# Kernel tuning notes

Measured on AMD Instinct MI355X. Metric: run time of the kernel, lower is better.

Reference implementation:

```python
import jax, jax.numpy as jnp
import numpy as np
from jax import lax

B, Z, X, Y = 8, 4, 32, 32
N = Z * X * Y
REAL_SIZE = jnp.array([25.0, 25.0, 4.0], dtype=jnp.float32)
THRESHOLD = 0.5
CUTOFF = 2.0


def setup_inputs() -> dict:
    key = jax.random.key(0)
    k1, k2 = jax.random.split(key)
    pred = jax.random.normal(k1, (B, Z, X, Y, 10), dtype=jnp.float32)
    targ = jax.random.uniform(k2, (B, Z, X, Y, 10), dtype=jnp.float32)
    return {"pred": pred, "targ": targ}


def _grid():
    z, x, y = jnp.meshgrid(jnp.arange(Z), jnp.arange(X), jnp.arange(Y), indexing="ij")
    return jnp.stack([z, x, y], -1).reshape(N, 3).astype(jnp.float32)


def _nms_mask(adj0, a0):
    # Fixed-size masked version of the original iterative suppression:
    # adj0: [N,N] bool, strictly-upper-triangular 'closer than cutoff' graph
    # a0:   [N] bool, currently active (above-threshold) points in conf-desc order
    def step(state):
        a, _ = state
        m = adj0 & a[:, None] & a[None, :]
        mf = m.astype(jnp.float32)
        r = mf.sum(0)                              # restrain_tensor = DIS.sum(0)
        r = r - (r != 0).astype(jnp.float32) @ mf  # subtract suppressed suppressors
        return ((r == 0.0) & a, a.sum())
    def cond(state):
        a, prev = state
        return a.sum() != prev
    a, _ = lax.while_loop(cond, step, (a0, jnp.int32(-1)))
    return a


def _per_batch(pd_conf, pd_pos, pd_R, tg_conf, tg_pos, tg_R):
    # pd_conf/tg_conf: [N]; pd_pos/tg_pos: [N,3] normalized; pd_R/tg_R: [N,3,3]
    pd_active = pd_conf > THRESHOLD
    tg_active = tg_conf > THRESHOLD
    # sort predictions by confidence descending, inactive pushed to the end
    skey = jnp.where(pd_active, pd_conf, -jnp.inf)
    order = jnp.argsort(-skey)
    pd_pos = pd_pos[order]
    pd_R = pd_R[order]
    a0 = pd_active[order]
    # NMS in NORMALIZED coordinates (as in the original module: real_size scaling
    # is applied only AFTER argnms)
    d = jnp.sqrt(jnp.sum((pd_pos[:, None, :] - pd_pos[None, :, :]) ** 2, -1))  # [N,N]
    iu = jnp.arange(N)
    adj0 = (d < CUTOFF) & (iu[:, None] < iu[None, :])
    keep = lax.stop_gradient(_nms_mask(adj0, a0))
    # greedy matching in real coordinates
    pd_r = pd_pos * REAL_SIZE
    tg_r = tg_pos * REAL_SIZE
    dist = jnp.sqrt(jnp.sum((tg_r[:, None, :] - pd_r[None, :, :]) ** 2, -1))  # [N_tg, N_pd]
    within = (dist < CUTOFF) & tg_active[:, None] & keep[None, :]
    has = within.any(0)                 # pred j has at least one target within cutoff
    first_tg = jnp.argmax(within, 0)    # first (lowest-index) matching target per pred
    tp = has.sum().astype(jnp.int32)
    n_pd = keep.sum().astype(jnp.int32)
    n_tg = tg_active.sum().astype(jnp.int32)
    cm = jnp.stack([tp, n_pd - tp, n_tg - tp])  # [matched, unmatched_pred, unmatched_targ]
    # mean rotation-angle error over matched pairs (3 rotation rows each)
    tgRm = tg_R[first_tg]  # [N,3,3]
    cos = jnp.sum(pd_R * tgRm, -1) / (
        jnp.linalg.norm(pd_R, axis=-1) * jnp.linalg.norm(tgRm, axis=-1))
    ang = jnp.arccos(jnp.clip(cos, -1.0, 1.0)) / jnp.pi * 180.0  # [N,3]
    w = has.astype(jnp.float32)[:, None]
    ms = jnp.where(tp > 0,
                   jnp.sum(ang * w) / (3.0 * jnp.maximum(tp, 1).astype(jnp.float32)),
                   0.0)
    return cm, ms


def _forward(pred, targ):
    grid = _grid()
    zxy = jnp.array([Z, X, Y], dtype=jnp.float32)
    def fields(t, is_pred):
        conf = jax.nn.sigmoid(t[..., 0]) if is_pred else t[..., 0]
        conf = conf.reshape(B, N)
        pos = (t[..., 1:4].reshape(B, N, 3) + grid) / zxy  # (off + cell_idx)/ZXY
        rx = t[..., 4:7].reshape(B, N, 3)
        ry = t[..., 7:10].reshape(B, N, 3)
        R = jnp.stack([rx, ry, jnp.cross(rx, ry)], axis=-2)  # [B,N,3,3]
        return conf, pos, R
    pc, pp, pR = fields(pred, True)
    tc, tpos, tR = fields(targ, False)
    cm, ms = jax.vmap(_per_batch)(pc, pp, pR, tc, tpos, tR)
    return cm.reshape(B, 1, 1, 3), ms.reshape(B, 1, 1, 1).astype(jnp.float32)


def reference(pred, targ):
    return _forward(pred, targ)
```

## Files before the change

### kernel.cpp

```cpp
#include <hip/hip_runtime.h>
#include <math.h>

#define NB    8
#define NPTS  4096
#define NTH   1024
#define SPT   4
#define NFILT 16
#define MAXQ  64
#define MAXU  256
#define MAXK  256

#define WS_PCNT 0
#define WS_TCNT 32
#define WS_PKEY 4096
#define WS_PPOS 266240
#define WS_TPOS 790528

__device__ __forceinline__ int blockReduceSumI(int v, int* scr, int tid) {
    #pragma unroll
    for (int o = 32; o > 0; o >>= 1) v += __shfl_down(v, o, 64);
    if ((tid & 63) == 0) scr[tid >> 6] = v;
    __syncthreads();
    if (tid == 0) {
        int s = 0;
        #pragma unroll
        for (int w = 0; w < NTH / 64; ++w) s += scr[w];
        scr[16] = s;
    }
    __syncthreads();
    return scr[16];
}

__device__ __forceinline__ float blockReduceSumF(float v, float* scr, int tid) {
    #pragma unroll
    for (int o = 32; o > 0; o >>= 1) v += __shfl_down(v, o, 64);
    if ((tid & 63) == 0) scr[tid >> 6] = v;
    __syncthreads();
    if (tid == 0) {
        float s = 0.0f;
        #pragma unroll
        for (int w = 0; w < NTH / 64; ++w) s += scr[w];
        scr[16] = s;
    }
    __syncthreads();
    return scr[16];
}

__device__ __forceinline__ float rowAngleDeg(float a0, float a1, float a2,
                                             float b0, float b1, float b2) {
    float dot = a0 * b0 + a1 * b1 + a2 * b2;
    float na = sqrtf(a0 * a0 + a1 * a1 + a2 * a2);
    float nb = sqrtf(b0 * b0 + b1 * b1 + b2 * b2);
    float c = dot / (na * nb);
    c = fminf(1.0f, fmaxf(-1.0f, c));
    return acosf(c) * 57.29577951308232f;
}

__global__ __launch_bounds__(256) void prep_kernel(const float* __restrict__ pred,
                                                   const float* __restrict__ targ,
                                                   unsigned char* __restrict__ ws) {
    __shared__ int lcnt;
    __shared__ int gbase;
    __shared__ int wbase[4];
    unsigned int* pcnt = (unsigned int*)(ws + WS_PCNT);
    unsigned int* tcnt = (unsigned int*)(ws + WS_TCNT);
    unsigned long long* pkey = (unsigned long long*)(ws + WS_PKEY);
    float4* ppos = (float4*)(ws + WS_PPOS);
    float4* tpos = (float4*)(ws + WS_TPOS);

    const int tid = threadIdx.x;
    const int g = blockIdx.x * 256 + tid;
    const int tensor = g >> 15;
    const int batch = (g >> 12) & 7;
    const int n = g & 4095;
    const float* base = (tensor ? targ : pred)
                        + (size_t)batch * NPTS * 10 + (size_t)n * 10;
    float2 f0 = *(const float2*)base;
    float2 f1 = *(const float2*)(base + 2);
    float gz = (float)(n >> 10);
    float gx = (float)((n >> 5) & 31);
    float gy = (float)(n & 31);

    bool active;
    unsigned long long key = 0;
    float4 rec;
    if (tensor == 0) {
        float conf = 1.0f / (1.0f + expf(-f0.x));
        active = conf > 0.5f;
        unsigned int u = ~(__float_as_uint(conf) | 0x80000000u);
        key = ((unsigned long long)u << 32) | (unsigned int)n;
        rec = make_float4((f0.y + gz) * 0.25f,
                          (f1.x + gx) * 0.03125f,
                          (f1.y + gy) * 0.03125f,
                          (float)n);
    } else {
        active = f0.x > 0.5f;
        rec = make_float4((f0.y + gz) * 0.25f * 25.0f,
                          (f1.x + gx) * 0.03125f * 25.0f,
                          (f1.y + gy) * 0.03125f * 4.0f,
                          (float)n);
    }

    if (tid == 0) lcnt = 0;
    __syncthreads();
    const int lane = tid & 63, wid = tid >> 6;
    unsigned long long ball = __ballot(active);
    int lofs = __popcll(ball & ((1ull << lane) - 1ull));
    if (lane == 0) wbase[wid] = atomicAdd(&lcnt, __popcll(ball));
    __syncthreads();
    if (tid == 0) {
        unsigned int* cp = tensor ? &tcnt[batch] : &pcnt[batch];
        gbase = (int)atomicAdd(cp, (unsigned int)lcnt);
    }
    __syncthreads();
    if (active) {
        int e = batch * NPTS + gbase + wbase[wid] + lofs;
        if (tensor == 0) { pkey[e] = key; ppos[e] = rec; }
        else tpos[e] = rec;
    }
}

__global__ __launch_bounds__(NTH) void molan_kernel(const float* __restrict__ pred,
                                                    const float* __restrict__ targ,
                                                    const unsigned char* __restrict__ ws,
                                                    float* __restrict__ out) {
    __shared__ int   scr_i[32];
    __shared__ float scr_f[32];
    __shared__ unsigned long long scr_m[16];
    __shared__ int   cnt[8];
    __shared__ unsigned long long f_key[NFILT];
    __shared__ float f_x[NFILT], f_y[NFILT], f_z[NFILT];
    __shared__ unsigned long long q_key[MAXQ];
    __shared__ float q_x[MAXQ], q_y[MAXQ], q_z[MAXQ];
    __shared__ unsigned long long u_key[MAXU];
    __shared__ float u_x[MAXU], u_y[MAXU], u_z[MAXU];
    __shared__ float k_x[MAXK], k_y[MAXK], k_z[MAXK];
    __shared__ int   k_idx[MAXK];
    __shared__ unsigned int k_match[MAXK];

    const int b = blockIdx.x;
    const int tid = threadIdx.x;
    const float* pb = pred + (size_t)b * NPTS * 10;
    const float* tb = targ + (size_t)b * NPTS * 10;
    const unsigned int* pcnt = (const unsigned int*)(ws + WS_PCNT);
    const unsigned int* tcnt = (const unsigned int*)(ws + WS_TCNT);
    const unsigned long long* pkey = (const unsigned long long*)(ws + WS_PKEY) + b * NPTS;
    const float4* ppos = (const float4*)(ws + WS_PPOS) + b * NPTS;
    const float4* tpos = (const float4*)(ws + WS_TPOS) + b * NPTS;
    const int np = (int)pcnt[b];
    const int nt = (int)tcnt[b];

    unsigned long long key[SPT];
    bool  act[SPT];
    int   pidx[SPT];
    float cx[SPT], cy[SPT], cz[SPT];
    #pragma unroll
    for (int s = 0; s < SPT; ++s) {
        int slot = tid + NTH * s;
        bool a = slot < np;
        act[s] = a;
        key[s] = a ? pkey[slot] : ~0ull;
        float4 p = a ? ppos[slot] : make_float4(0.f, 0.f, 0.f, 0.f);
        cx[s] = p.x; cy[s] = p.y; cz[s] = p.z; pidx[s] = (int)p.w;
    }
    bool  t_act[SPT];
    int   t_n[SPT];
    float t_x[SPT], t_y[SPT], t_z[SPT];
    #pragma unroll
    for (int s = 0; s < SPT; ++s) {
        int slot = tid + NTH * s;
        bool a = slot < nt;
        t_act[s] = a;
        float4 p = a ? tpos[slot] : make_float4(0.f, 0.f, 0.f, 0.f);
        t_x[s] = p.x; t_y[s] = p.y; t_z[s] = p.z; t_n[s] = (int)p.w;
    }

    int cur = np;
    int prev = -1;
    while (cur != prev) {
        {
            unsigned long long bk = ~0ull;
            float bx = 0.f, by = 0.f, bz = 0.f;
            #pragma unroll
            for (int s = 0; s < SPT; ++s)
                if (act[s] && key[s] < bk) { bk = key[s]; bx = cx[s]; by = cy[s]; bz = cz[s]; }
            #pragma unroll
            for (int o = 32; o > 0; o >>= 1) {
                unsigned long long ok = __shfl_xor(bk, o, 64);
                float ox = __shfl_xor(bx, o, 64);
                float oy = __shfl_xor(by, o, 64);
                float oz = __shfl_xor(bz, o, 64);
                if (ok < bk) { bk = ok; bx = ox; by = oy; bz = oz; }
            }
            if ((tid & 63) == 0) {
                int w = tid >> 6;
                f_key[w] = bk; f_x[w] = bx; f_y[w] = by; f_z[w] = bz;
            }
        }
        __syncthreads();

        bool sflag[SPT], pend[SPT];
        #pragma unroll
        for (int s = 0; s < SPT; ++s) {
            sflag[s] = false; pend[s] = false;
            if (!act[s]) continue;
            bool found = false;
            for (int f = 0; f < NFILT; ++f) {
                if (f_key[f] < key[s]) {
                    float dx = f_x[f] - cx[s], dy = f_y[f] - cy[s], dz = f_z[f] - cz[s];
                    if (dx * dx + dy * dy + dz * dz < 4.0f) { found = true; break; }
                }
            }
            if (found) sflag[s] = true;
            else pend[s] = true;
        }
        while (true) {
            if (tid == 0) cnt[1] = 0;
            __syncthreads();
            int qe[SPT];
            #pragma unroll
            for (int s = 0; s < SPT; ++s) {
                qe[s] = -1;
                if (pend[s]) {
                    int e = atomicAdd(&cnt[1], 1);
                    if (e < MAXQ) {
                        q_key[e] = key[s]; q_x[e] = cx[s]; q_y[e] = cy[s]; q_z[e] = cz[s];
                        qe[s] = e; pend[s] = false;
                    }
                }
            }
            __syncthreads();
            if (cnt[1] == 0) break;
            const int Q = min(cnt[1], MAXQ);
            unsigned long long mask = 0;
            for (int e = 0; e < Q; ++e) {
                unsigned long long qk = q_key[e];
                float qx = q_x[e], qy = q_y[e], qz = q_z[e];
                bool hit = false;
                #pragma unroll
                for (int s = 0; s < SPT; ++s) {
                    if (act[s] && key[s] < qk) {
                        float dx = cx[s] - qx, dy = cy[s] - qy, dz = cz[s] - qz;
                        if (dx * dx + dy * dy + dz * dz < 4.0f) hit = true;
                    }
                }
                if (hit) mask |= (1ull << e);
            }
            #pragma unroll
            for (int o = 32; o > 0; o >>= 1) mask |= __shfl_xor(mask, o, 64);
            if ((tid & 63) == 0) scr_m[tid >> 6] = mask;
            __syncthreads();
            unsigned long long full = 0;
            #pragma unroll
            for (int w = 0; w < NTH / 64; ++w) full |= scr_m[w];
            #pragma unroll
            for (int s = 0; s < SPT; ++s)
                if (qe[s] >= 0) sflag[s] = (full >> qe[s]) & 1ull;
        }

        bool upend[SPT], supp[SPT];
        #pragma unroll
        for (int s = 0; s < SPT; ++s) {
            upend[s] = act[s] && !sflag[s];
            supp[s] = false;
        }
        while (true) {
            if (tid == 0) cnt[2] = 0;
            __syncthreads();
            #pragma unroll
            for (int s = 0; s < SPT; ++s) {
                if (upend[s]) {
                    int e = atomicAdd(&cnt[2], 1);
                    if (e < MAXU) {
                        u_key[e] = key[s]; u_x[e] = cx[s]; u_y[e] = cy[s]; u_z[e] = cz[s];
                        upend[s] = false;
                    }
                }
            }
            __syncthreads();
            if (cnt[2] == 0) break;
            const int Ku = min(cnt[2], MAXU);
            #pragma unroll
            for (int s = 0; s < SPT; ++s) {
                if (!act[s] || supp[s]) continue;
                for (int e = 0; e < Ku; ++e) {
                    if (u_key[e] < key[s]) {
                        float dx = u_x[e] - cx[s], dy = u_y[e] - cy[s], dz = u_z[e] - cz[s];
                        if (dx * dx + dy * dy + dz * dz < 4.0f) { supp[s] = true; break; }
                    }
                }
            }
        }
        int loc = 0;
        #pragma unroll
        for (int s = 0; s < SPT; ++s) {
            if (act[s] && supp[s]) act[s] = false;
            loc += act[s] ? 1 : 0;
        }
        prev = cur;
        cur = blockReduceSumI(loc, scr_i, tid);
    }
    const int n_pd = cur;

    bool kpend[SPT];
    #pragma unroll
    for (int s = 0; s < SPT; ++s) kpend[s] = act[s];
    int loc_tp = 0;
    float loc_ang = 0.0f;
    while (true) {
        if (tid == 0) cnt[3] = 0;
        __syncthreads();
        #pragma unroll
        for (int s = 0; s < SPT; ++s) {
            if (kpend[s]) {
                int e = atomicAdd(&cnt[3], 1);
                if (e < MAXK) {
                    k_x[e] = cx[s] * 25.0f; k_y[e] = cy[s] * 25.0f; k_z[e] = cz[s] * 4.0f;
                    k_idx[e] = pidx[s];
                    k_match[e] = 0xFFFFFFFFu;
                    kpend[s] = false;
                }
            }
        }
        __syncthreads();
        if (cnt[3] == 0) break;
        const int K = min(cnt[3], MAXK);
        #pragma unroll
        for (int s = 0; s < SPT; ++s) {
            if (!t_act[s]) continue;
            float tx = t_x[s], ty = t_y[s], tz = t_z[s];
            for (int e = 0; e < K; ++e) {
                float dx = tx - k_x[e], dy = ty - k_y[e], dz = tz - k_z[e];
                if (dx * dx + dy * dy + dz * dz < 4.0f)
                    atomicMin(&k_match[e], (unsigned int)t_n[s]);
            }
        }
        __syncthreads();
        if (tid < K) {
            unsigned int m = k_match[tid];
            if (m != 0xFFFFFFFFu) {
                ++loc_tp;
                const float2* pr = (const float2*)(pb + (size_t)k_idx[tid] * 10 + 4);
                float2 p0 = pr[0], p1 = pr[1], p2v = pr[2];
                float ax0 = p0.x, ax1 = p0.y, ax2 = p1.x;
                float ay0 = p1.y, ay1 = p2v.x, ay2 = p2v.y;
                float az0 = ax1 * ay2 - ax2 * ay1;
                float az1 = ax2 * ay0 - ax0 * ay2;
                float az2 = ax0 * ay1 - ax1 * ay0;
                const float2* tr = (const float2*)(tb + (size_t)m * 10 + 4);
                float2 t0 = tr[0], t1 = tr[1], t2v = tr[2];
                float bx0 = t0.x, bx1 = t0.y, bx2 = t1.x;
                float by0 = t1.y, by1 = t2v.x, by2 = t2v.y;
                float bz0 = bx1 * by2 - bx2 * by1;
                float bz1 = bx2 * by0 - bx0 * by2;
                float bz2 = bx0 * by1 - bx1 * by0;
                loc_ang += rowAngleDeg(ax0, ax1, ax2, bx0, bx1, bx2);
                loc_ang += rowAngleDeg(ay0, ay1, ay2, by0, by1, by2);
                loc_ang += rowAngleDeg(az0, az1, az2, bz0, bz1, bz2);
            }
        }
    }

    int tp = blockReduceSumI(loc_tp, scr_i, tid);
    float angsum = blockReduceSumF(loc_ang, scr_f, tid);

    if (tid == 0) {
        out[b * 3 + 0] = (float)tp;
        out[b * 3 + 1] = (float)(n_pd - tp);
        out[b * 3 + 2] = (float)(nt - tp);
        out[NB * 3 + b] = (tp > 0) ? (angsum / (3.0f * (float)tp)) : 0.0f;
    }
}

extern "C" void kernel_launch(void* const* d_in, const int* in_sizes, int n_in,
                              void* d_out, int out_size, void* d_ws, size_t ws_size,
                              hipStream_t stream) {
    const float* pred = (const float*)d_in[0];
    const float* targ = (const float*)d_in[1];
    float* out = (float*)d_out;
    unsigned char* ws = (unsigned char*)d_ws;
    hipMemsetAsync(ws, 0, 64, stream);
    prep_kernel<<<dim3(256), dim3(256), 0, stream>>>(pred, targ, ws);
    molan_kernel<<<dim3(NB), dim3(NTH), 0, stream>>>(pred, targ, ws, out);
}
```

Measured before the change: 79.34 us.

## Replace global atomic compaction with per-chunk counts and drop the memset

The prep kernel now writes per-256-point chunk counts instead of atomically appending to global per-batch counters, so the separate memset launch and the atomics go away. The main kernel reads the 16 chunk counts per batch and treats slots as a sparse chunked layout rather than a dense prefix. It also raises the query buffer size, replaces the ballot mask reduction with a shared result array, and turns the batch loops into do-while loops that exit after a single pass when counts fit, saving barriers. The cost is that the main kernel now scans the full sparse 4096-slot layout.

```diff
diff --git a/kernel.cpp b/kernel.cpp
--- a/kernel.cpp
+++ b/kernel.cpp
@@ -6,15 +6,15 @@
 #define NTH   1024
 #define SPT   4
 #define NFILT 16
-#define MAXQ  64
+#define MAXQ  512
 #define MAXU  256
 #define MAXK  256
 
-#define WS_PCNT 0
-#define WS_TCNT 32
-#define WS_PKEY 4096
-#define WS_PPOS 266240
-#define WS_TPOS 790528
+#define WS_PCC  0
+#define WS_TCC  512
+#define WS_PKEY 1024
+#define WS_PPOS 263168
+#define WS_TPOS 787456
 
 __device__ __forceinline__ int blockReduceSumI(int v, int* scr, int tid) {
     #pragma unroll
@@ -59,20 +59,19 @@
 __global__ __launch_bounds__(256) void prep_kernel(const float* __restrict__ pred,
                                                    const float* __restrict__ targ,
                                                    unsigned char* __restrict__ ws) {
-    __shared__ int lcnt;
-    __shared__ int gbase;
-    __shared__ int wbase[4];
-    unsigned int* pcnt = (unsigned int*)(ws + WS_PCNT);
-    unsigned int* tcnt = (unsigned int*)(ws + WS_TCNT);
+    __shared__ int wcnt[4];
+    unsigned int* pcc = (unsigned int*)(ws + WS_PCC);
+    unsigned int* tcc = (unsigned int*)(ws + WS_TCC);
     unsigned long long* pkey = (unsigned long long*)(ws + WS_PKEY);
     float4* ppos = (float4*)(ws + WS_PPOS);
     float4* tpos = (float4*)(ws + WS_TPOS);
 
     const int tid = threadIdx.x;
-    const int g = blockIdx.x * 256 + tid;
-    const int tensor = g >> 15;
-    const int batch = (g >> 12) & 7;
-    const int n = g & 4095;
+    const int blk = blockIdx.x;
+    const int tensor = blk >> 7;
+    const int batch = (blk >> 4) & 7;
+    const int chunk = blk & 15;
+    const int n = chunk * 256 + tid;
     const float* base = (tensor ? targ : pred)
                         + (size_t)batch * NPTS * 10 + (size_t)n * 10;
     float2 f0 = *(const float2*)base;
@@ -101,20 +100,19 @@
                           (float)n);
     }
 
-    if (tid == 0) lcnt = 0;
-    __syncthreads();
     const int lane = tid & 63, wid = tid >> 6;
     unsigned long long ball = __ballot(active);
     int lofs = __popcll(ball & ((1ull << lane) - 1ull));
-    if (lane == 0) wbase[wid] = atomicAdd(&lcnt, __popcll(ball));
-    __syncthreads();
+    if (lane == 0) wcnt[wid] = __popcll(ball);
+    __syncthreads();
+    int wb = 0;
+    for (int w = 0; w < wid; ++w) wb += wcnt[w];
     if (tid == 0) {
-        unsigned int* cp = tensor ? &tcnt[batch] : &pcnt[batch];
-        gbase = (int)atomicAdd(cp, (unsigned int)lcnt);
-    }
-    __syncthreads();
+        unsigned int t = (unsigned int)(wcnt[0] + wcnt[1] + wcnt[2] + wcnt[3]);
+        (tensor ? tcc : pcc)[batch * 16 + chunk] = t;
+    }
     if (active) {
-        int e = batch * NPTS + gbase + wbase[wid] + lofs;
+        int e = batch * NPTS + chunk * 256 + wb + lofs;
         if (tensor == 0) { pkey[e] = key; ppos[e] = rec; }
         else tpos[e] = rec;
     }
@@ -126,12 +124,13 @@
                                                     float* __restrict__ out) {
     __shared__ int   scr_i[32];
     __shared__ float scr_f[32];
-    __shared__ unsigned long long scr_m[16];
-    __shared__ int   cnt[8];
+    __shared__ int   cnt[4];
+    __shared__ int   ccP[16], ccT[16];
     __shared__ unsigned long long f_key[NFILT];
     __shared__ float f_x[NFILT], f_y[NFILT], f_z[NFILT];
     __shared__ unsigned long long q_key[MAXQ];
     __shared__ float q_x[MAXQ], q_y[MAXQ], q_z[MAXQ];
+    __shared__ int   q_res[MAXQ];
     __shared__ unsigned long long u_key[MAXU];
     __shared__ float u_x[MAXU], u_y[MAXU], u_z[MAXU];
     __shared__ float k_x[MAXK], k_y[MAXK], k_z[MAXK];
@@ -142,13 +141,13 @@
     const int tid = threadIdx.x;
     const float* pb = pred + (size_t)b * NPTS * 10;
     const float* tb = targ + (size_t)b * NPTS * 10;
-    const unsigned int* pcnt = (const unsigned int*)(ws + WS_PCNT);
-    const unsigned int* tcnt = (const unsigned int*)(ws + WS_TCNT);
     const unsigned long long* pkey = (const unsigned long long*)(ws + WS_PKEY) + b * NPTS;
     const float4* ppos = (const float4*)(ws + WS_PPOS) + b * NPTS;
     const float4* tpos = (const float4*)(ws + WS_TPOS) + b * NPTS;
-    const int np = (int)pcnt[b];
-    const int nt = (int)tcnt[b];
+
+    if (tid < 16) ccP[tid] = (int)((const unsigned int*)(ws + WS_PCC))[b * 16 + tid];
+    else if (tid < 32) ccT[tid - 16] = (int)((const unsigned int*)(ws + WS_TCC))[b * 16 + tid - 16];
+    __syncthreads();
 
     unsigned long long key[SPT];
     bool  act[SPT];
@@ -157,11 +156,15 @@
     #pragma unroll
     for (int s = 0; s < SPT; ++s) {
         int slot = tid + NTH * s;
-        bool a = slot < np;
+        bool a = (slot & 255) < ccP[slot >> 8];
         act[s] = a;
-        key[s] = a ? pkey[slot] : ~0ull;
-        float4 p = a ? ppos[slot] : make_float4(0.f, 0.f, 0.f, 0.f);
-        cx[s] = p.x; cy[s] = p.y; cz[s] = p.z; pidx[s] = (int)p.w;
+        key[s] = ~0ull;
+        cx[s] = cy[s] = cz[s] = 0.f; pidx[s] = 0;
+        if (a) {
+            key[s] = pkey[slot];
+            float4 p = ppos[slot];
+            cx[s] = p.x; cy[s] = p.y; cz[s] = p.z; pidx[s] = (int)p.w;
+        }
     }
     bool  t_act[SPT];
     int   t_n[SPT];
@@ -169,13 +172,19 @@
     #pragma unroll
     for (int s = 0; s < SPT; ++s) {
         int slot = tid + NTH * s;
-        bool a = slot < nt;
+        bool a = (slot & 255) < ccT[slot >> 8];
         t_act[s] = a;
-        float4 p = a ? tpos[slot] : make_float4(0.f, 0.f, 0.f, 0.f);
-        t_x[s] = p.x; t_y[s] = p.y; t_z[s] = p.z; t_n[s] = (int)p.w;
-    }
-
-    int cur = np;
+        t_x[s] = t_y[s] = t_z[s] = 0.f; t_n[s] = 0;
+        if (a) {
+            float4 p = tpos[slot];
+            t_x[s] = p.x; t_y[s] = p.y; t_z[s] = p.z; t_n[s] = (int)p.w;
+        }
+    }
+
+    int loc = 0;
+    #pragma unroll
+    for (int s = 0; s < SPT; ++s) loc += act[s] ? 1 : 0;
+    int cur = blockReduceSumI(loc, scr_i, tid);
     int prev = -1;
     while (cur != prev) {
         {
@@ -214,7 +223,7 @@
             if (found) sflag[s] = true;
             else pend[s] = true;
         }
-        while (true) {
+        do {
             if (tid == 0) cnt[1] = 0;
             __syncthreads();
             int qe[SPT];
@@ -225,14 +234,13 @@
                     int e = atomicAdd(&cnt[1], 1);
                     if (e < MAXQ) {
                         q_key[e] = key[s]; q_x[e] = cx[s]; q_y[e] = cy[s]; q_z[e] = cz[s];
+                        q_res[e] = 0;
                         qe[s] = e; pend[s] = false;
                     }
                 }
             }
             __syncthreads();
-            if (cnt[1] == 0) break;
             const int Q = min(cnt[1], MAXQ);
-            unsigned long long mask = 0;
             for (int e = 0; e < Q; ++e) {
                 unsigned long long qk = q_key[e];
                 float qx = q_x[e], qy = q_y[e], qz = q_z[e];
@@ -244,19 +252,13 @@
                         if (dx * dx + dy * dy + dz * dz < 4.0f) hit = true;
                     }
                 }
-                if (hit) mask |= (1ull << e);
-            }
-            #pragma unroll
-            for (int o = 32; o > 0; o >>= 1) mask |= __shfl_xor(mask, o, 64);
-            if ((tid & 63) == 0) scr_m[tid >> 6] = mask;
-            __syncthreads();
-            unsigned long long full = 0;
-            #pragma unroll
-            for (int w = 0; w < NTH / 64; ++w) full |= scr_m[w];
+                if (hit) q_res[e] = 1;
+            }
+            __syncthreads();
             #pragma unroll
             for (int s = 0; s < SPT; ++s)
-                if (qe[s] >= 0) sflag[s] = (full >> qe[s]) & 1ull;
-        }
+                if (qe[s] >= 0) sflag[s] = (q_res[qe[s]] != 0);
+        } while (cnt[1] > MAXQ);
 
         bool upend[SPT], supp[SPT];
         #pragma unroll
@@ -264,7 +266,7 @@
             upend[s] = act[s] && !sflag[s];
             supp[s] = false;
         }
-        while (true) {
+        do {
             if (tid == 0) cnt[2] = 0;
             __syncthreads();
             #pragma unroll
@@ -278,7 +280,6 @@
                 }
             }
             __syncthreads();
-            if (cnt[2] == 0) break;
             const int Ku = min(cnt[2], MAXU);
             #pragma unroll
             for (int s = 0; s < SPT; ++s) {
@@ -290,8 +291,8 @@
                     }
                 }
             }
-        }
-        int loc = 0;
+        } while (cnt[2] > MAXU);
+        loc = 0;
         #pragma unroll
         for (int s = 0; s < SPT; ++s) {
             if (act[s] && supp[s]) act[s] = false;
@@ -307,7 +308,7 @@
     for (int s = 0; s < SPT; ++s) kpend[s] = act[s];
     int loc_tp = 0;
     float loc_ang = 0.0f;
-    while (true) {
+    do {
         if (tid == 0) cnt[3] = 0;
         __syncthreads();
         #pragma unroll
@@ -323,7 +324,6 @@
             }
         }
         __syncthreads();
-        if (cnt[3] == 0) break;
         const int K = min(cnt[3], MAXK);
         #pragma unroll
         for (int s = 0; s < SPT; ++s) {
@@ -359,12 +359,15 @@
                 loc_ang += rowAngleDeg(az0, az1, az2, bz0, bz1, bz2);
             }
         }
-    }
+    } while (cnt[3] > MAXK);
 
     int tp = blockReduceSumI(loc_tp, scr_i, tid);
     float angsum = blockReduceSumF(loc_ang, scr_f, tid);
 
     if (tid == 0) {
+        int nt = 0;
+        #pragma unroll
+        for (int i = 0; i < 16; ++i) nt += ccT[i];
         out[b * 3 + 0] = (float)tp;
         out[b * 3 + 1] = (float)(n_pd - tp);
         out[b * 3 + 2] = (float)(nt - tp);
@@ -379,7 +382,6 @@
     const float* targ = (const float*)d_in[1];
     float* out = (float*)d_out;
     unsigned char* ws = (unsigned char*)d_ws;
-    hipMemsetAsync(ws, 0, 64, stream);
     prep_kernel<<<dim3(256), dim3(256), 0, stream>>>(pred, targ, ws);
     molan_kernel<<<dim3(NB), dim3(NTH), 0, stream>>>(pred, targ, ws, out);
 }
```

Result: faster. 76.18 us (-4.0%).
